# Performance work log

Hardware: AMD Instinct MI355X
Metric: run time of the kernel (lower is better)

Reference implementation:

```python
import jax, jax.numpy as jnp
import numpy as np

G_CRYSTALS = 64   # number of crystals in the batch
N_ATOMS = 64      # atoms per crystal (dense n^2 edge block per crystal)
N_HEADS = 8
HEAD_DIM = 64


def _make_edges(g, n):
    # dense all-pairs (i, j) within each crystal; atoms of crystal c occupy [c*n, (c+1)*n)
    base = np.arange(g, dtype=np.int32)[:, None, None] * n   # (G,1,1)
    idx = np.arange(n, dtype=np.int32)
    e0 = np.broadcast_to(base + idx[None, :, None], (g, n, n)).reshape(-1)  # query index
    e1 = np.broadcast_to(base + idx[None, None, :], (g, n, n)).reshape(-1)  # key index
    return jnp.asarray(np.stack([e0, e1], axis=0))  # (2, M)


def setup_inputs() -> dict:
    key = jax.random.key(0)
    k0, k1, k2, k3, k4 = jax.random.split(key, 5)
    N = G_CRYSTALS * N_ATOMS                 # 4096 atoms total
    M = G_CRYSTALS * N_ATOMS * N_ATOMS       # 262144 edges
    q = jax.random.normal(k0, (N, N_HEADS, HEAD_DIM), jnp.float32)
    k = jax.random.normal(k1, (N, N_HEADS, HEAD_DIM), jnp.float32)
    v = jax.random.normal(k2, (N, N_HEADS, HEAD_DIM), jnp.float32)
    attn_weights = jax.random.normal(k3, (M, N_HEADS), jnp.float32)          # per-edge additive bias
    values = jax.random.normal(k4, (M, N_HEADS, HEAD_DIM), jnp.float32) * 0.1  # per-edge fused value term
    edges = _make_edges(G_CRYSTALS, N_ATOMS)
    return {"q": q, "k": k, "v": v, "attn_weights": attn_weights,
            "values": values, "edges": edges}


def reference(q, k, v, attn_weights, values, edges):
    # Faithful to the norm_func_mode==0 ('default') fallback path of
    # _scaled_dot_product_attention: per-edge logits, softmax over keys per
    # query (within each crystal's dense block), fused value term.
    N, H, Dh = q.shape
    e0, e1 = edges[0], edges[1]
    scale = 1.0 / jnp.sqrt(jnp.asarray(Dh, q.dtype))
    # per-edge attention logits: (M, H)
    a = jnp.einsum('mhd,mhd->mh', q[e0] * scale, k[e1]) + attn_weights
    # stable softmax over edges sharing the same query index e0
    m = jax.ops.segment_max(a, e0, num_segments=N)      # (N, H)
    p = jnp.exp(a - m[e0])                              # (M, H)
    denom = jax.ops.segment_sum(p, e0, num_segments=N)  # (N, H)
    w = p / denom[e0]                                   # (M, H)
    # output[i] = sum_j w[ij] * (v[j] + values[ij])
    out = jax.ops.segment_sum(w[:, :, None] * (v[e1] + values), e0, num_segments=N)
    return out  # (N, H, Dh)
```

## Files before the change

### kernel.cpp

```cpp
#include <hip/hip_runtime.h>


#define NH 8
#define HD 64
#define ROWSTRIDE 68

__global__ __launch_bounds__(256, 3)
void softmax_kernel(const float* __restrict__ q,
                    const float* __restrict__ k,
                    const float* __restrict__ aw,
                    float* __restrict__ w_out) {
    const int c = blockIdx.x & 63;
    const int h = blockIdx.x >> 6;
    const int t = threadIdx.x;

    __shared__ __align__(16) float sq[64][ROWSTRIDE];
    __shared__ __align__(16) float sk[64][ROWSTRIDE];
    __shared__ __align__(16) float sa[64][ROWSTRIDE];

    {
        const size_t rowbase = ((size_t)c * 64) * (NH * HD) + (size_t)h * HD;
        const float* qg = q + rowbase;
        const float* kg = k + rowbase;
        #pragma unroll
        for (int s = 0; s < 4; ++s) {
            int u   = t + 256 * s;
            int row = u >> 4;
            int col = (u & 15) * 4;
            size_t goff = (size_t)row * (NH * HD) + col;
            *(float4*)&sq[row][col] = *(const float4*)(qg + goff);
            *(float4*)&sk[row][col] = *(const float4*)(kg + goff);
        }
        const float* ag = aw + ((size_t)c * 4096) * NH + h;
        #pragma unroll
        for (int s = 0; s < 16; ++s) {
            int idx = t + 256 * s;
            sa[idx >> 6][idx & 63] = ag[(size_t)idx * NH];
        }
    }
    __syncthreads();

    {
        const int wv = t >> 6;
        const int i  = t & 63;
        const int jbase = wv * 16;
        float acc[16];
        #pragma unroll
        for (int jj = 0; jj < 16; ++jj) acc[jj] = 0.f;
        #pragma unroll 4
        for (int d4 = 0; d4 < 16; ++d4) {
            float4 qv = *(const float4*)&sq[i][d4 * 4];
            #pragma unroll
            for (int jj = 0; jj < 16; ++jj) {
                float4 kv = *(const float4*)&sk[jbase + jj][d4 * 4];
                acc[jj] += qv.x * kv.x + qv.y * kv.y + qv.z * kv.z + qv.w * kv.w;
            }
        }
        #pragma unroll
        for (int jj = 0; jj < 16; ++jj)
            sa[i][jbase + jj] = acc[jj] * 0.125f + sa[i][jbase + jj];
    }
    __syncthreads();

    {
        const int r  = t >> 2;
        const int jb = (t & 3) * 16;
        float p[16];
        float mx = -1e30f;
        #pragma unroll
        for (int jj = 0; jj < 16; ++jj) { p[jj] = sa[r][jb + jj]; mx = fmaxf(mx, p[jj]); }
        mx = fmaxf(mx, __shfl_xor(mx, 1));
        mx = fmaxf(mx, __shfl_xor(mx, 2));
        float sum = 0.f;
        #pragma unroll
        for (int jj = 0; jj < 16; ++jj) { p[jj] = __expf(p[jj] - mx); sum += p[jj]; }
        sum += __shfl_xor(sum, 1);
        sum += __shfl_xor(sum, 2);
        const float inv = 1.0f / sum;
        float* wg = w_out + ((size_t)(c * NH + h)) * 4096 + r * 64 + jb;
        #pragma unroll
        for (int s = 0; s < 4; ++s) {
            float4 o = make_float4(p[4*s] * inv, p[4*s+1] * inv,
                                   p[4*s+2] * inv, p[4*s+3] * inv);
            *(float4*)(wg + 4 * s) = o;
        }
    }
}

__global__ __launch_bounds__(256, 8)
void stream_kernel(const float* __restrict__ v,
                   const float* __restrict__ values,
                   const float* __restrict__ w_in,
                   float* __restrict__ out) {
    const int c = blockIdx.x & 63;
    const int i = blockIdx.x >> 6;
    const int t = threadIdx.x;

    __shared__ float sw[NH][64];
    __shared__ float sred[4][512];

    #pragma unroll
    for (int s = 0; s < 2; ++s) {
        int idx = t + 256 * s;
        sw[idx >> 6][idx & 63] =
            w_in[((size_t)(c * NH) + (idx >> 6)) * 4096 + i * 64 + (idx & 63)];
    }
    __syncthreads();

    const int ww = t >> 6;
    const int l  = t & 63;
    const int jbase = ww * 16;
    const int h0 = l >> 4;
    const float* valbase = values + ((size_t)(c * 4096 + i * 64 + jbase)) * 512;
    const float* vbase   = v      + ((size_t)(c * 64 + jbase)) * 512;

    float4 acc0 = make_float4(0.f, 0.f, 0.f, 0.f);
    float4 acc1 = make_float4(0.f, 0.f, 0.f, 0.f);
    #pragma unroll 4
    for (int jj = 0; jj < 16; ++jj) {
        const size_t ro = (size_t)jj * 512 + 4 * l;
        float4 a0 = *(const float4*)(valbase + ro);
        float4 a1 = *(const float4*)(valbase + ro + 256);
        float4 b0 = *(const float4*)(vbase + ro);
        float4 b1 = *(const float4*)(vbase + ro + 256);
        float w0 = sw[h0][jbase + jj];
        float w1 = sw[h0 + 4][jbase + jj];
        acc0.x += w0 * (b0.x + a0.x); acc0.y += w0 * (b0.y + a0.y);
        acc0.z += w0 * (b0.z + a0.z); acc0.w += w0 * (b0.w + a0.w);
        acc1.x += w1 * (b1.x + a1.x); acc1.y += w1 * (b1.y + a1.y);
        acc1.z += w1 * (b1.z + a1.z); acc1.w += w1 * (b1.w + a1.w);
    }
    *(float4*)&sred[ww][4 * l]       = acc0;
    *(float4*)&sred[ww][256 + 4 * l] = acc1;
    __syncthreads();

    float* ob = out + ((size_t)(c * 64 + i)) * 512;
    #pragma unroll
    for (int s = 0; s < 2; ++s) {
        int d = t + 256 * s;
        ob[d] = sred[0][d] + sred[1][d] + sred[2][d] + sred[3][d];
    }
}

extern "C" void kernel_launch(void* const* d_in, const int* in_sizes, int n_in,
                              void* d_out, int out_size, void* d_ws, size_t ws_size,
                              hipStream_t stream) {
    const float* q      = (const float*)d_in[0];
    const float* k      = (const float*)d_in[1];
    const float* v      = (const float*)d_in[2];
    const float* aw     = (const float*)d_in[3];
    const float* values = (const float*)d_in[4];
    float* out = (float*)d_out;
    float* w_ws = (float*)d_ws;

    hipLaunchKernelGGL(softmax_kernel, dim3(512), dim3(256), 0, stream,
                       q, k, aw, w_ws);
    hipLaunchKernelGGL(stream_kernel, dim3(4096), dim3(256), 0, stream,
                       v, values, w_ws, out);
}
```

Measured before the change: 730.8 us.

## Compute w·v in the softmax kernel and stream only per-edge values

```diff
diff --git a/kernel.cpp b/kernel.cpp
--- a/kernel.cpp
+++ b/kernel.cpp
@@ -2,36 +2,40 @@
 
 
 #define NH 8
-#define HD 64
-#define ROWSTRIDE 68
+#define RS 68
 
-__global__ __launch_bounds__(256, 3)
-void softmax_kernel(const float* __restrict__ q,
-                    const float* __restrict__ k,
-                    const float* __restrict__ aw,
-                    float* __restrict__ w_out) {
+__global__ __launch_bounds__(256, 2)
+void softmax_wv_kernel(const float* __restrict__ q,
+                       const float* __restrict__ k,
+                       const float* __restrict__ v,
+                       const float* __restrict__ aw,
+                       float* __restrict__ w_out,
+                       float* __restrict__ part_out) {
     const int c = blockIdx.x & 63;
     const int h = blockIdx.x >> 6;
     const int t = threadIdx.x;
 
-    __shared__ __align__(16) float sq[64][ROWSTRIDE];
-    __shared__ __align__(16) float sk[64][ROWSTRIDE];
-    __shared__ __align__(16) float sa[64][ROWSTRIDE];
+    __shared__ __align__(16) float sq[64][RS];
+    __shared__ __align__(16) float sk[64][RS];
+    __shared__ __align__(16) float sv[64][RS];
+    __shared__ __align__(16) float sa[64][RS];
 
     {
-        const size_t rowbase = ((size_t)c * 64) * (NH * HD) + (size_t)h * HD;
+        const size_t rowbase = ((size_t)(c * 64)) * 512 + (size_t)h * 64;
         const float* qg = q + rowbase;
         const float* kg = k + rowbase;
+        const float* vg = v + rowbase;
         #pragma unroll
         for (int s = 0; s < 4; ++s) {
             int u   = t + 256 * s;
             int row = u >> 4;
             int col = (u & 15) * 4;
-            size_t goff = (size_t)row * (NH * HD) + col;
+            size_t goff = (size_t)row * 512 + col;
             *(float4*)&sq[row][col] = *(const float4*)(qg + goff);
             *(float4*)&sk[row][col] = *(const float4*)(kg + goff);
+            *(float4*)&sv[row][col] = *(const float4*)(vg + goff);
         }
-        const float* ag = aw + ((size_t)c * 4096) * NH + h;
+        const float* ag = aw + ((size_t)(c * 4096)) * NH + h;
         #pragma unroll
         for (int s = 0; s < 16; ++s) {
             int idx = t + 256 * s;
@@ -82,22 +86,48 @@
         for (int s = 0; s < 4; ++s) {
             float4 o = make_float4(p[4*s] * inv, p[4*s+1] * inv,
                                    p[4*s+2] * inv, p[4*s+3] * inv);
+            sa[r][jb + 4*s]     = o.x; sa[r][jb + 4*s + 1] = o.y;
+            sa[r][jb + 4*s + 2] = o.z; sa[r][jb + 4*s + 3] = o.w;
             *(float4*)(wg + 4 * s) = o;
+        }
+    }
+    __syncthreads();
+
+    {
+        const int dq = t & 15;
+        const int ig = t >> 4;
+        float4 acc[4];
+        #pragma unroll
+        for (int r = 0; r < 4; ++r) acc[r] = make_float4(0.f, 0.f, 0.f, 0.f);
+        #pragma unroll 4
+        for (int j = 0; j < 64; ++j) {
+            float4 vv = *(const float4*)&sv[j][4 * dq];
+            #pragma unroll
+            for (int r = 0; r < 4; ++r) {
+                float p = sa[ig + 16 * r][j];
+                acc[r].x += p * vv.x; acc[r].y += p * vv.y;
+                acc[r].z += p * vv.z; acc[r].w += p * vv.w;
+            }
+        }
+        #pragma unroll
+        for (int r = 0; r < 4; ++r) {
+            const int i = ig + 16 * r;
+            *(float4*)&part_out[((size_t)(c * 64 + i)) * 512 + h * 64 + 4 * dq] = acc[r];
         }
     }
 }
 
 __global__ __launch_bounds__(256, 8)
-void stream_kernel(const float* __restrict__ v,
-                   const float* __restrict__ values,
+void stream_kernel(const float* __restrict__ values,
                    const float* __restrict__ w_in,
+                   const float* __restrict__ part_in,
                    float* __restrict__ out) {
     const int c = blockIdx.x & 63;
     const int i = blockIdx.x >> 6;
     const int t = threadIdx.x;
 
-    __shared__ float sw[NH][64];
-    __shared__ float sred[4][512];
+    __shared__ float sw[NH][65];
+    __shared__ __align__(16) float sred[2][512];
 
     #pragma unroll
     for (int s = 0; s < 2; ++s) {
@@ -107,38 +137,31 @@
     }
     __syncthreads();
 
-    const int ww = t >> 6;
-    const int l  = t & 63;
-    const int jbase = ww * 16;
-    const int h0 = l >> 4;
-    const float* valbase = values + ((size_t)(c * 4096 + i * 64 + jbase)) * 512;
-    const float* vbase   = v      + ((size_t)(c * 64 + jbase)) * 512;
+    const int slot = t & 127;
+    const int half = t >> 7;
+    const int h    = slot >> 4;
+    const float* vp = values + ((size_t)(c * 4096 + i * 64 + half * 32)) * 512 + 4 * slot;
 
-    float4 acc0 = make_float4(0.f, 0.f, 0.f, 0.f);
-    float4 acc1 = make_float4(0.f, 0.f, 0.f, 0.f);
-    #pragma unroll 4
-    for (int jj = 0; jj < 16; ++jj) {
-        const size_t ro = (size_t)jj * 512 + 4 * l;
-        float4 a0 = *(const float4*)(valbase + ro);
-        float4 a1 = *(const float4*)(valbase + ro + 256);
-        float4 b0 = *(const float4*)(vbase + ro);
-        float4 b1 = *(const float4*)(vbase + ro + 256);
-        float w0 = sw[h0][jbase + jj];
-        float w1 = sw[h0 + 4][jbase + jj];
-        acc0.x += w0 * (b0.x + a0.x); acc0.y += w0 * (b0.y + a0.y);
-        acc0.z += w0 * (b0.z + a0.z); acc0.w += w0 * (b0.w + a0.w);
-        acc1.x += w1 * (b1.x + a1.x); acc1.y += w1 * (b1.y + a1.y);
-        acc1.z += w1 * (b1.z + a1.z); acc1.w += w1 * (b1.w + a1.w);
+    float4 acc = make_float4(0.f, 0.f, 0.f, 0.f);
+    #pragma unroll 8
+    for (int jj = 0; jj < 32; ++jj) {
+        float4 a = *(const float4*)vp;
+        float  w = sw[h][half * 32 + jj];
+        acc.x += w * a.x; acc.y += w * a.y;
+        acc.z += w * a.z; acc.w += w * a.w;
+        vp += 512;
     }
-    *(float4*)&sred[ww][4 * l]       = acc0;
-    *(float4*)&sred[ww][256 + 4 * l] = acc1;
+    *(float4*)&sred[half][4 * slot] = acc;
     __syncthreads();
 
-    float* ob = out + ((size_t)(c * 64 + i)) * 512;
-    #pragma unroll
-    for (int s = 0; s < 2; ++s) {
-        int d = t + 256 * s;
-        ob[d] = sred[0][d] + sred[1][d] + sred[2][d] + sred[3][d];
+    if (t < 128) {
+        float4 r0 = *(float4*)&sred[0][4 * t];
+        float4 r1 = *(float4*)&sred[1][4 * t];
+        const size_t ob = ((size_t)(c * 64 + i)) * 512 + 4 * t;
+        float4 pp = *(const float4*)(part_in + ob);
+        float4 o  = make_float4(r0.x + r1.x + pp.x, r0.y + r1.y + pp.y,
+                                r0.z + r1.z + pp.z, r0.w + r1.w + pp.w);
+        *(float4*)(out + ob) = o;
     }
 }
 
@@ -150,11 +173,12 @@
     const float* v      = (const float*)d_in[2];
     const float* aw     = (const float*)d_in[3];
     const float* values = (const float*)d_in[4];
-    float* out = (float*)d_out;
+    float* out  = (float*)d_out;
     float* w_ws = (float*)d_ws;
+    float* part = (float*)d_ws + (size_t)64 * NH * 4096;
 
-    hipLaunchKernelGGL(softmax_kernel, dim3(512), dim3(256), 0, stream,
-                       q, k, aw, w_ws);
+    hipLaunchKernelGGL(softmax_wv_kernel, dim3(512), dim3(256), 0, stream,
+                       q, k, v, aw, w_ws, part);
     hipLaunchKernelGGL(stream_kernel, dim3(4096), dim3(256), 0, stream,
-                       v, values, w_ws, out);
+                       values, w_ws, part, out);
 }
```

After: 720.8 us. About the same (-1.4%).
